# Kernel tuning notes

Measured on AMD Instinct MI355X. Metric: run time of the kernel, lower is better.

## Reference

```python
import jax, jax.numpy as jnp
import numpy as np

TOKENS = 512
DIM_HEAD = 64
MAX_TOKENS = 2000
HEADS = 8
BATCH = 8


def _build_indices(tokens: int, max_tokens: int) -> np.ndarray:
    # Faithful replication of the torch index construction (done once in numpy).
    idx = np.arange(-tokens, tokens + 1)
    pad = max_tokens - 2 * tokens + 1
    row = np.concatenate([np.full(pad, idx[0]), idx, np.full(pad, idx[-1])])
    mat = np.stack([np.roll(row, i) for i in range(max_tokens)])
    mat = mat[: max_tokens - tokens + 2, max_tokens - tokens + 1 :]
    # torch fancy indexing wraps negative indices -> take mod of table size
    return (mat % (2 * tokens - 1)).astype(np.int32)


def setup_inputs() -> dict:
    key = jax.random.key(0)
    kq, kp = jax.random.split(key)
    scale = DIM_HEAD ** (-0.5)
    q = jax.random.normal(kq, (BATCH, HEADS, TOKENS, DIM_HEAD), dtype=jnp.float32)
    rel_pos_emb = (
        jax.random.normal(kp, (HEADS, 2 * TOKENS - 1, DIM_HEAD), dtype=jnp.float32)
        * scale
    )
    indices = jnp.asarray(_build_indices(TOKENS, MAX_TOKENS))
    return {"q": q, "rel_pos_emb": rel_pos_emb, "indices": indices}


def reference(q, rel_pos_emb, indices):
    t = q.shape[2]
    idx = indices[:t, :t]  # [r, t]
    # gather: [heads, r, t, dim_head]
    gathered = rel_pos_emb[:, idx]
    # emb[b,h,t,r] = sum_d q[b,h,t,d] * gathered[h,r,t,d]
    return jnp.einsum("bhtd,hrtd->bhtr", q, gathered)
```

## Files before the change

kernel.cpp:

```cpp
#include <hip/hip_runtime.h>


#define TOKENS 512
#define DIMH 64
#define NREL 1023
#define IDXN 1490
#define PSTR 132

typedef short bf16x8 __attribute__((ext_vector_type(8)));
typedef float f32x4 __attribute__((ext_vector_type(4)));

__device__ __forceinline__ short f2bf(float x) {
    unsigned u = __float_as_uint(x);
    return (short)((u + 0x7FFFu + ((u >> 16) & 1u)) >> 16);
}
__device__ __forceinline__ bf16x8 cvt8(float4 a, float4 b) {
    bf16x8 r;
    r[0] = f2bf(a.x); r[1] = f2bf(a.y); r[2] = f2bf(a.z); r[3] = f2bf(a.w);
    r[4] = f2bf(b.x); r[5] = f2bf(b.y); r[6] = f2bf(b.z); r[7] = f2bf(b.w);
    return r;
}

__global__ __launch_bounds__(256, 4)
void relpos_mfma2(const float* __restrict__ q,
                  const float* __restrict__ emb,
                  const int* __restrict__ indices,
                  float* __restrict__ out)
{
    __shared__ float Ps[64 * PSTR];

    const int tid = threadIdx.x;
    const int blk = blockIdx.x;
    const int rh = blk & 1;
    const int tt = (blk >> 1) & 7;
    const int bh = blk >> 4;
    const int h  = bh & 7;
    const int t0 = tt * 64;

    const int lane = tid & 63;
    const int wave = tid >> 6;
    const int quad = lane >> 4;
    const int l15  = lane & 15;

    bf16x8 af[4][2];
    {
        const float* qb = q + ((size_t)bh * TOKENS + t0 + l15) * DIMH + quad * 8;
#pragma unroll
        for (int mi = 0; mi < 4; ++mi) {
            const float* p0 = qb + (size_t)mi * 16 * DIMH;
            float4 a0 = *(const float4*)p0;
            float4 a1 = *(const float4*)(p0 + 4);
            float4 b0 = *(const float4*)(p0 + 32);
            float4 b1 = *(const float4*)(p0 + 36);
            af[mi][0] = cvt8(a0, a1);
            af[mi][1] = cvt8(b0, b1);
        }
    }

    const float* embh = emb + (size_t)h * NREL * DIMH;
    const int v4 = (tid & 15) * 4;
    const int u0 = tid >> 4;

    for (int rt = 0; rt < 4; ++rt) {
        const int r0 = rh * 256 + rt * 64;
        const int j_a = indices[(size_t)(r0 + 63) * IDXN + t0];

        bf16x8 bf[2][2];
#pragma unroll
        for (int nn = 0; nn < 2; ++nn) {
            int j = j_a + (2 * wave + nn) * 16 + l15;
            if (j >= NREL) j -= NREL;
            const float* ep = embh + (size_t)j * DIMH + quad * 8;
            float4 a0 = *(const float4*)ep;
            float4 a1 = *(const float4*)(ep + 4);
            float4 b0 = *(const float4*)(ep + 32);
            float4 b1 = *(const float4*)(ep + 36);
            bf[nn][0] = cvt8(a0, a1);
            bf[nn][1] = cvt8(b0, b1);
        }

        __syncthreads();

#pragma unroll
        for (int nn = 0; nn < 2; ++nn) {
            const int nb = (2 * wave + nn) * 16 + l15;
#pragma unroll
            for (int mi = 0; mi < 4; ++mi) {
                f32x4 acc = {0.f, 0.f, 0.f, 0.f};
                acc = __builtin_amdgcn_mfma_f32_16x16x32_bf16(af[mi][0], bf[nn][0], acc, 0, 0, 0);
                acc = __builtin_amdgcn_mfma_f32_16x16x32_bf16(af[mi][1], bf[nn][1], acc, 0, 0, 0);
                float* pw = Ps + (size_t)(mi * 16 + quad * 4) * PSTR + nb;
#pragma unroll
                for (int rg = 0; rg < 4; ++rg) pw[rg * PSTR] = acc[rg];
            }
        }

        __syncthreads();

        float* op = out + ((size_t)bh * TOKENS + t0 + u0) * (size_t)TOKENS + r0 + v4;
#pragma unroll
        for (int p = 0; p < 4; ++p) {
            const int u = u0 + p * 16;
            const int base = u - v4 + 63;
            const float* pr = Ps + (size_t)u * PSTR;
            float4 o;
            o.x = pr[base];
            o.y = pr[base - 1];
            o.z = pr[base - 2];
            o.w = pr[base - 3];
            *(float4*)(op + (size_t)p * 16 * TOKENS) = o;
        }
    }
}

extern "C" void kernel_launch(void* const* d_in, const int* in_sizes, int n_in,
                              void* d_out, int out_size, void* d_ws, size_t ws_size,
                              hipStream_t stream) {
    const float* q       = (const float*)d_in[0];
    const float* emb     = (const float*)d_in[1];
    const int*   indices = (const int*)d_in[2];
    float* out = (float*)d_out;

    relpos_mfma2<<<dim3(1024), dim3(256), 0, stream>>>(q, emb, indices, out);
}
```

Measured before the change: 105.1 us.

## Write MFMA results directly to global memory, dropping shared-memory skew staging

Removes the LDS staging buffer and both barriers per tile. Each MFMA accumulator element is now written straight to its skewed output position, with a range check selecting which results fall inside the 64-wide output window. The index lookups are also hoisted out of the loop. This saves the LDS round trip and the synchronisation, but the global writes become scattered scalar stores along diagonals instead of coalesced float4 rows, and about half the computed values are discarded.

New measurement: 114.4 us. 1.09x slower.

```diff
diff --git a/kernel.cpp b/kernel.cpp
--- a/kernel.cpp
+++ b/kernel.cpp
@@ -5,7 +5,6 @@
 #define DIMH 64
 #define NREL 1023
 #define IDXN 1490
-#define PSTR 132
 
 typedef short bf16x8 __attribute__((ext_vector_type(8)));
 typedef float f32x4 __attribute__((ext_vector_type(4)));
@@ -22,13 +21,11 @@
 }
 
 __global__ __launch_bounds__(256, 4)
-void relpos_mfma2(const float* __restrict__ q,
-                  const float* __restrict__ emb,
-                  const int* __restrict__ indices,
-                  float* __restrict__ out)
+void relpos_direct(const float* __restrict__ q,
+                   const float* __restrict__ emb,
+                   const int* __restrict__ indices,
+                   float* __restrict__ out)
 {
-    __shared__ float Ps[64 * PSTR];
-
     const int tid = threadIdx.x;
     const int blk = blockIdx.x;
     const int rh = blk & 1;
@@ -57,58 +54,48 @@
         }
     }
 
+    int ja[4];
+#pragma unroll
+    for (int rt = 0; rt < 4; ++rt)
+        ja[rt] = indices[(size_t)(rh * 256 + rt * 64 + 63) * IDXN + t0];
+
     const float* embh = emb + (size_t)h * NREL * DIMH;
-    const int v4 = (tid & 15) * 4;
-    const int u0 = tid >> 4;
+    const int nb0 = wave * 32 + l15;
+
+    float* outq = out + ((size_t)bh * TOKENS + t0) * (size_t)TOKENS
+                + rh * 256 + 63 + quad * 4 * 513 - nb0;
 
     for (int rt = 0; rt < 4; ++rt) {
-        const int r0 = rh * 256 + rt * 64;
-        const int j_a = indices[(size_t)(r0 + 63) * IDXN + t0];
-
-        bf16x8 bf[2][2];
+        bf16x8 bfr[2][2];
 #pragma unroll
         for (int nn = 0; nn < 2; ++nn) {
-            int j = j_a + (2 * wave + nn) * 16 + l15;
+            int j = ja[rt] + nb0 + nn * 16;
             if (j >= NREL) j -= NREL;
             const float* ep = embh + (size_t)j * DIMH + quad * 8;
             float4 a0 = *(const float4*)ep;
             float4 a1 = *(const float4*)(ep + 4);
             float4 b0 = *(const float4*)(ep + 32);
             float4 b1 = *(const float4*)(ep + 36);
-            bf[nn][0] = cvt8(a0, a1);
-            bf[nn][1] = cvt8(b0, b1);
+            bfr[nn][0] = cvt8(a0, a1);
+            bfr[nn][1] = cvt8(b0, b1);
         }
 
-        __syncthreads();
-
+        float* outr = outq + rt * 64;
 #pragma unroll
         for (int nn = 0; nn < 2; ++nn) {
-            const int nb = (2 * wave + nn) * 16 + l15;
+            const int nbq = quad * 4 - (nb0 + nn * 16) + 63;
 #pragma unroll
             for (int mi = 0; mi < 4; ++mi) {
                 f32x4 acc = {0.f, 0.f, 0.f, 0.f};
-                acc = __builtin_amdgcn_mfma_f32_16x16x32_bf16(af[mi][0], bf[nn][0], acc, 0, 0, 0);
-                acc = __builtin_amdgcn_mfma_f32_16x16x32_bf16(af[mi][1], bf[nn][1], acc, 0, 0, 0);
-                float* pw = Ps + (size_t)(mi * 16 + quad * 4) * PSTR + nb;
+                acc = __builtin_amdgcn_mfma_f32_16x16x32_bf16(af[mi][0], bfr[nn][0], acc, 0, 0, 0);
+                acc = __builtin_amdgcn_mfma_f32_16x16x32_bf16(af[mi][1], bfr[nn][1], acc, 0, 0, 0);
 #pragma unroll
-                for (int rg = 0; rg < 4; ++rg) pw[rg * PSTR] = acc[rg];
+                for (int rg = 0; rg < 4; ++rg) {
+                    const int v = nbq + mi * 16 + rg;
+                    if ((unsigned)v < 64u)
+                        outr[(size_t)(mi * 16 + rg) * 513 - nn * 16] = acc[rg];
+                }
             }
-        }
-
-        __syncthreads();
-
-        float* op = out + ((size_t)bh * TOKENS + t0 + u0) * (size_t)TOKENS + r0 + v4;
-#pragma unroll
-        for (int p = 0; p < 4; ++p) {
-            const int u = u0 + p * 16;
-            const int base = u - v4 + 63;
-            const float* pr = Ps + (size_t)u * PSTR;
-            float4 o;
-            o.x = pr[base];
-            o.y = pr[base - 1];
-            o.z = pr[base - 2];
-            o.w = pr[base - 3];
-            *(float4*)(op + (size_t)p * 16 * TOKENS) = o;
         }
     }
 }
@@ -121,5 +108,5 @@
     const int*   indices = (const int*)d_in[2];
     float* out = (float*)d_out;
 
-    relpos_mfma2<<<dim3(1024), dim3(256), 0, stream>>>(q, emb, indices, out);
+    relpos_direct<<<dim3(1024), dim3(256), 0, stream>>>(q, emb, indices, out);
 }
```
